# Optimization experiments

Measured on AMD Instinct MI355X. Metric: run time of the kernel, lower is better.

Reference implementation:

```python
import jax, jax.numpy as jnp
import numpy as np

B, IC, ID, OC, OD = 8, 8, 16, 8, 16   # batch, in_caps, in_dim, out_caps, out_dim
H = W = 32
K, STRIDE, PAD = 3, 1, 1
ITER = 3
EPS_BN = 1e-5
EPS_SQ = 1e-8


def p4convp4(x, w, stride, pad):
    """Group-equivariant P4->P4 conv.
    x: (N, Cin, 4, H, W); w: (Cout, Cin, 4, k, k) -> (N, Cout, 4, H', W').
    Output-rotation-r filter: input group axis rolled by r, spatial kernel rotated by r*90deg.
    """
    Cout, Cin, _, kh, kw = w.shape
    tw = jnp.stack(
        [jnp.rot90(jnp.roll(w, r, axis=2), k=r, axes=(3, 4)) for r in range(4)], axis=1
    )  # (Cout, 4, Cin, 4, k, k)
    tw = tw.reshape(Cout * 4, Cin * 4, kh, kw)
    N, _, _, Hh, Ww = x.shape
    xf = x.reshape(N, Cin * 4, Hh, Ww)
    y = jax.lax.conv_general_dilated(
        xf, tw, (stride, stride), [(pad, pad), (pad, pad)],
        dimension_numbers=("NCHW", "OIHW", "NCHW"))
    return y.reshape(N, Cout, 4, y.shape[2], y.shape[3])


def batchnorm3d(x, gamma, beta):
    # x: (N, C, D, H, W); training-mode batch stats over (N, D, H, W) per channel
    mean = x.mean(axis=(0, 2, 3, 4), keepdims=True)
    var = x.var(axis=(0, 2, 3, 4), keepdims=True)
    g = gamma.reshape(1, -1, 1, 1, 1)
    b = beta.reshape(1, -1, 1, 1, 1)
    return (x - mean) * jax.lax.rsqrt(var + EPS_BN) * g + b


def squash(s, axis):
    norm = jnp.linalg.norm(s, axis=axis, keepdims=True)
    scale = norm ** 2 / (1 + norm ** 2) / (norm + EPS_SQ)
    return scale * s


def setup_inputs() -> dict:
    key = jax.random.key(0)
    k1, k2 = jax.random.split(key)
    in_capsules = jax.random.normal(k1, (B, IC, ID, 4, H, W), jnp.float32)
    w = jax.random.normal(k2, (OC * OD, ID, 4, K, K), jnp.float32) * 0.05
    gamma = jnp.ones((OC * OD,), jnp.float32)
    beta = jnp.zeros((OC * OD,), jnp.float32)
    return {"in_capsules": in_capsules, "w": w, "gamma": gamma, "beta": beta}


def reference(in_capsules, w, gamma, beta):
    bsz = in_capsules.shape[0]
    x = in_capsules.reshape(bsz * IC, ID, 4, H, W)
    p = p4convp4(x, w, STRIDE, PAD)              # (B*IC, OC*OD, 4, H', W')
    p = batchnorm3d(p, gamma, beta)
    Hh, Ww = p.shape[-2], p.shape[-1]
    preds = p.reshape(bsz, IC, OC, OD, 4, Hh, Ww)

    b_ij = jnp.zeros((bsz, IC, OC, 1, 4, Hh, Ww), preds.dtype)
    c_ij = None
    v_j = None
    for it in range(ITER):
        c_ij = jax.nn.softmax(b_ij, axis=2)                      # over out_caps
        s_j = (c_ij * preds).sum(axis=1, keepdims=True)          # over in_caps
        v_j = squash(s_j, axis=3)                                # over out_dim
        if it < ITER - 1:
            b_ij = b_ij + (preds * v_j).sum(axis=3, keepdims=True)

    c = jnp.squeeze(c_ij, axis=3)                                # (B, IC, OC, 4, H', W')
    # normalized categorical entropy over out_caps
    ent = -(c * jnp.log(c)).sum(axis=2) / jnp.log(jnp.float32(OC))  # (B, IC, 4, H', W')
    entropy = ent.mean(axis=(1, 2, 3, 4)).sum()
    return (jnp.squeeze(v_j, axis=1), entropy)
```

## Files before the change

kernel.cpp:

```cpp
#include <hip/hip_runtime.h>
#include <hip/hip_bf16.h>


typedef short bf16x8 __attribute__((ext_vector_type(8)));
typedef float f32x4 __attribute__((ext_vector_type(4)));
typedef unsigned int u32x2 __attribute__((ext_vector_type(2)));

__device__ inline float bf2f(unsigned int u) {
    union { unsigned int i; float f; } x;
    x.i = u << 16;
    return x.f;
}
__device__ inline unsigned short f2bf(float f) {
    union { float f; unsigned int u; } x;
    x.f = f;
    unsigned int r = x.u + 0x7fffu + ((x.u >> 16) & 1u);
    return (unsigned short)(r >> 16);
}

__device__ inline float dppx1(float x) {
    return __int_as_float(__builtin_amdgcn_update_dpp(0, __float_as_int(x), 0xB1, 0xF, 0xF, false));
}
__device__ inline float dppx2(float x) {
    return __int_as_float(__builtin_amdgcn_update_dpp(0, __float_as_int(x), 0x4E, 0xF, 0xF, false));
}
template <int PATT>
__device__ inline float swzf(float x) {
    return __int_as_float(__builtin_amdgcn_ds_swizzle(__float_as_int(x), PATT));
}
#define SWZ4  0x101F
#define SWZ8  0x201F
#define SWZ16 0x401F
__device__ inline float psum32(float x) {
    u32x2 r = __builtin_amdgcn_permlane32_swap(__float_as_uint(x), __float_as_uint(x), false, false);
    return __uint_as_float(r[0]) + __uint_as_float(r[1]);
}

__global__ __launch_bounds__(256) void k_twb(const float* __restrict__ w,
                                             unsigned short* __restrict__ twb) {
    int idx = blockIdx.x * 256 + threadIdx.x;
    int tap = idx >> 15;
    int rem = idx & 32767;
    int co4 = rem >> 6;
    int cst = rem & 63;
    int ci = cst ^ ((co4 & 7) << 3);
    int r = co4 & 3, co = co4 >> 2;
    int s = ci & 3, cicap = ci >> 2;
    int ky = tap / 3, kx = tap % 3;
    int sy, sx;
    switch (r) {
        case 0: sy = ky;      sx = kx;      break;
        case 1: sy = kx;      sx = 2 - ky;  break;
        case 2: sy = 2 - ky;  sx = 2 - kx;  break;
        default: sy = 2 - kx; sx = ky;      break;
    }
    int ss = (s - r) & 3;
    twb[idx] = f2bf(w[(((co * 16 + cicap) * 4 + ss) * 3 + sy) * 3 + sx]);
}

__global__ __launch_bounds__(256) void k_prep(const float* __restrict__ xf,
                                              unsigned short* __restrict__ xpad) {
    int n = blockIdx.x >> 5, y = blockIdx.x & 31;
    int tid = threadIdx.x;
    __shared__ float tile[64][33];
#pragma unroll
    for (int it = 0; it < 8; ++it) {
        int ci = it * 8 + (tid >> 5), x = tid & 31;
        tile[ci][x] = xf[((n * 64 + ci) * 32 + y) * 32 + x];
    }
    __syncthreads();
    int xx = 1 + (tid >> 3), g = tid & 7;
    int x = xx - 1;
    int lg = g ^ (xx & 7);
    unsigned short vals[8];
#pragma unroll
    for (int j = 0; j < 8; ++j) vals[j] = f2bf(tile[lg * 8 + j][x]);
    uint4 pk;
    pk.x = (unsigned)vals[0] | ((unsigned)vals[1] << 16);
    pk.y = (unsigned)vals[2] | ((unsigned)vals[3] << 16);
    pk.z = (unsigned)vals[4] | ((unsigned)vals[5] << 16);
    pk.w = (unsigned)vals[6] | ((unsigned)vals[7] << 16);
    *reinterpret_cast<uint4*>(&xpad[(n * 34 + (y + 1)) * 2176 + xx * 64 + g * 8]) = pk;
}

__global__ __launch_bounds__(256) void k_mconv(const unsigned short* __restrict__ xpad,
                                               const unsigned short* __restrict__ twb,
                                               unsigned short* __restrict__ p) {
    int n = blockIdx.x, yt = blockIdx.y, cot = blockIdx.z;
    int y0 = yt * 4;
    int tid = threadIdx.x, lane = tid & 63, wave = tid >> 6;
    int wm = (wave >> 1) * 64, wn = (wave & 1) * 64;
    int p15 = lane & 15, hi = lane >> 4;

    __shared__ unsigned short xs[6 * 34 * 64];
    __shared__ unsigned short wA[128 * 64];

    {
        const uint4* src = reinterpret_cast<const uint4*>(xpad + (n * 34 + y0) * 2176);
        uint4* dst = reinterpret_cast<uint4*>(xs);
        for (int t = tid; t < 1632; t += 256) dst[t] = src[t];
    }

    f32x4 acc[4][4];
#pragma unroll
    for (int mf = 0; mf < 4; ++mf)
#pragma unroll
        for (int nf = 0; nf < 4; ++nf) acc[mf][nf] = (f32x4){0.f, 0.f, 0.f, 0.f};

    int yl[4], xb[4];
#pragma unroll
    for (int nf = 0; nf < 4; ++nf) {
        int posl = wn + nf * 16 + p15;
        yl[nf] = posl >> 5;
        xb[nf] = posl & 31;
    }

    for (int tap = 0; tap < 9; ++tap) {
        __syncthreads();
        {
            const uint4* wsrc = reinterpret_cast<const uint4*>(twb + (tap * 512 + cot * 128) * 64);
            uint4* wdst = reinterpret_cast<uint4*>(wA);
            for (int t = tid; t < 1024; t += 256) wdst[t] = wsrc[t];
        }
        __syncthreads();

        int ky = tap / 3, kx = tap % 3;

        bf16x8 a[4][2], b[4][2];
#pragma unroll
        for (int mf = 0; mf < 4; ++mf) {
            int co4l = wm + mf * 16 + p15;
#pragma unroll
            for (int s = 0; s < 2; ++s) {
                int cig = hi + s * 4;
                a[mf][s] = *reinterpret_cast<const bf16x8*>(
                    &wA[co4l * 64 + ((cig ^ (co4l & 7)) << 3)]);
            }
        }
#pragma unroll
        for (int nf = 0; nf < 4; ++nf) {
            int row = yl[nf] + ky, col = xb[nf] + kx;
#pragma unroll
            for (int s = 0; s < 2; ++s) {
                int cig = hi + s * 4;
                b[nf][s] = *reinterpret_cast<const bf16x8*>(
                    &xs[(row * 34 + col) * 64 + ((cig ^ (col & 7)) << 3)]);
            }
        }
#pragma unroll
        for (int s = 0; s < 2; ++s)
#pragma unroll
            for (int mf = 0; mf < 4; ++mf)
#pragma unroll
                for (int nf = 0; nf < 4; ++nf)
                    acc[mf][nf] = __builtin_amdgcn_mfma_f32_16x16x32_bf16(
                        a[mf][s], b[nf][s], acc[mf][nf], 0, 0, 0);
    }

#pragma unroll
    for (int mf = 0; mf < 4; ++mf)
#pragma unroll
        for (int nf = 0; nf < 4; ++nf) {
            int posl = wn + nf * 16 + p15;
            int y = y0 + (posl >> 5), x = posl & 31;
#pragma unroll
            for (int reg = 0; reg < 4; ++reg) {
                int co4 = cot * 128 + wm + mf * 16 + hi * 4 + reg;
                p[((n * 512 + co4) * 32 + y) * 32 + x] = f2bf(acc[mf][nf][reg]);
            }
        }
}

__global__ __launch_bounds__(256) void k_stats1(const unsigned short* __restrict__ pp,
                                                float* __restrict__ ps) {
    int c = blockIdx.x >> 2, q = blockIdx.x & 3;
    int tid = threadIdx.x;
    float s = 0.f, s2 = 0.f;
    for (int t = tid; t < 8192; t += 256) {
        int idx8 = t << 3;
        int nn = (q << 4) + (idx8 >> 12);
        int rem = idx8 & 4095;
        int co4 = (c << 2) + (rem >> 10);
        int pos = rem & 1023;
        uint4 d = *reinterpret_cast<const uint4*>(pp + (((nn << 9) + co4) << 10) + pos);
        float f;
        f = bf2f(d.x & 0xffffu); s += f; s2 += f * f;
        f = bf2f(d.x >> 16);     s += f; s2 += f * f;
        f = bf2f(d.y & 0xffffu); s += f; s2 += f * f;
        f = bf2f(d.y >> 16);     s += f; s2 += f * f;
        f = bf2f(d.z & 0xffffu); s += f; s2 += f * f;
        f = bf2f(d.z >> 16);     s += f; s2 += f * f;
        f = bf2f(d.w & 0xffffu); s += f; s2 += f * f;
        f = bf2f(d.w >> 16);     s += f; s2 += f * f;
    }
#pragma unroll
    for (int m = 1; m < 64; m <<= 1) {
        s  += __shfl_xor(s, m);
        s2 += __shfl_xor(s2, m);
    }
    __shared__ float rs[4], rs2[4];
    int wave = tid >> 6, lane = tid & 63;
    if (lane == 0) { rs[wave] = s; rs2[wave] = s2; }
    __syncthreads();
    if (tid == 0) {
        ps[blockIdx.x * 2]     = rs[0] + rs[1] + rs[2] + rs[3];
        ps[blockIdx.x * 2 + 1] = rs2[0] + rs2[1] + rs2[2] + rs2[3];
    }
}

__global__ __launch_bounds__(128) void k_ab(const float* __restrict__ ps,
                                            const float* __restrict__ gamma,
                                            const float* __restrict__ beta,
                                            float* __restrict__ ab) {
    int c = threadIdx.x;
    float S  = ps[(c * 4 + 0) * 2] + ps[(c * 4 + 1) * 2] + ps[(c * 4 + 2) * 2] + ps[(c * 4 + 3) * 2];
    float S2 = ps[(c * 4 + 0) * 2 + 1] + ps[(c * 4 + 1) * 2 + 1] + ps[(c * 4 + 2) * 2 + 1] + ps[(c * 4 + 3) * 2 + 1];
    float mean = S * (1.f / 262144.f);
    float var = S2 * (1.f / 262144.f) - mean * mean;
    float A = gamma[c] * rsqrtf(var + 1e-5f);
    ab[2 * c] = A;
    ab[2 * c + 1] = beta[c] - mean * A;
}

__global__ __launch_bounds__(256, 4) void k_route(const unsigned short* __restrict__ pp,
                                                  const float* __restrict__ ab,
                                                  float* __restrict__ out,
                                                  float* __restrict__ ent_out) {
    int bid = blockIdx.x;
    int u = ((bid >> 4) << 3) + (bid & 7);
    int ch = (bid >> 3) & 1;
    int y = u & 31, r = (u >> 5) & 3, b = u >> 7;
    int x0 = ch * 16;
    int tid = threadIdx.x;
    int wave = tid >> 6, lane = tid & 63;
    int i_l = lane >> 3, oc_l = lane & 7;

    __shared__ unsigned int Tl2[16][8][64];
    __shared__ unsigned short vst[8][16][18];
    __shared__ float ered[4];

#pragma unroll
    for (int t4i = 0; t4i < 4; ++t4i) {
        int t4 = tid + t4i * 256;
        int od = t4 >> 6, ls = t4 & 63;
        int ii = ls >> 3, oo = ls & 7;
        int c = oo * 16 + od;
        int co4 = c * 4 + r;
        int n = b * 8 + ii;
        float A = ab[2 * c], Bv = ab[2 * c + 1];
        const uint4* src = reinterpret_cast<const uint4*>(pp + ((n * 512 + co4) * 32 + y) * 32 + x0);
        uint4 d0 = src[0], d1 = src[1];
        unsigned wds[8] = {d0.x, d0.y, d0.z, d0.w, d1.x, d1.y, d1.z, d1.w};
#pragma unroll
        for (int j = 0; j < 8; ++j) {
            float tlo = A * bf2f(wds[j] & 0xffffu) + Bv;
            float thi = A * bf2f(wds[j] >> 16) + Bv;
            Tl2[od][j][ls] = (unsigned)f2bf(tlo) | ((unsigned)f2bf(thi) << 16);
        }
    }
    __syncthreads();

    float e_acc = 0.f;

    for (int q = 0; q < 2; ++q) {
        int p2 = wave + q * 4;
        float t0[16], t1[16];
#pragma unroll
        for (int od = 0; od < 16; ++od) {
            unsigned pr = Tl2[od][p2][lane];
            t0[od] = bf2f(pr & 0xffffu);
            t1[od] = bf2f(pr >> 16);
        }

        float b0 = 0.f, b1 = 0.f, c0, c1, sc0 = 0.f, sc1 = 0.f;
        float s0[16], s1[16];
        for (int it = 0; it < 3; ++it) {
            float m0 = b0, m1 = b1;
            m0 = fmaxf(m0, dppx1(m0));      m1 = fmaxf(m1, dppx1(m1));
            m0 = fmaxf(m0, dppx2(m0));      m1 = fmaxf(m1, dppx2(m1));
            m0 = fmaxf(m0, swzf<SWZ4>(m0)); m1 = fmaxf(m1, swzf<SWZ4>(m1));
            float e0 = __expf(b0 - m0), e1 = __expf(b1 - m1);
            float se0 = e0, se1 = e1;
            se0 += dppx1(se0);      se1 += dppx1(se1);
            se0 += dppx2(se0);      se1 += dppx2(se1);
            se0 += swzf<SWZ4>(se0); se1 += swzf<SWZ4>(se1);
            c0 = e0 * __builtin_amdgcn_rcpf(se0);
            c1 = e1 * __builtin_amdgcn_rcpf(se1);
            float n20 = 0.f, n21 = 0.f;
#pragma unroll
            for (int od = 0; od < 16; ++od) {
                float v0 = c0 * t0[od], v1 = c1 * t1[od];
                v0 += swzf<SWZ8>(v0);   v1 += swzf<SWZ8>(v1);
                v0 += swzf<SWZ16>(v0);  v1 += swzf<SWZ16>(v1);
                v0 = psum32(v0);        v1 = psum32(v1);
                s0[od] = v0;            s1[od] = v1;
                n20 += v0 * v0;         n21 += v1 * v1;
            }
            float nr0 = sqrtf(n20), nr1 = sqrtf(n21);
            sc0 = n20 * __builtin_amdgcn_rcpf((1.f + n20) * (nr0 + 1e-8f));
            sc1 = n21 * __builtin_amdgcn_rcpf((1.f + n21) * (nr1 + 1e-8f));
            if (it < 2) {
                float a0 = 0.f, a1 = 0.f;
#pragma unroll
                for (int od = 0; od < 16; ++od) {
                    a0 += t0[od] * s0[od];
                    a1 += t1[od] * s1[od];
                }
                b0 += a0 * sc0;
                b1 += a1 * sc1;
            }
        }
        e_acc += -c0 * __logf(c0) - c1 * __logf(c1);
        if (i_l == 0) {
#pragma unroll
            for (int od = 0; od < 16; ++od) {
                vst[oc_l][od][2 * p2]     = f2bf(sc0 * s0[od]);
                vst[oc_l][od][2 * p2 + 1] = f2bf(sc1 * s1[od]);
            }
        }
    }

    e_acc += dppx1(e_acc);
    e_acc += dppx2(e_acc);
    e_acc += swzf<SWZ4>(e_acc);
    e_acc += swzf<SWZ8>(e_acc);
    e_acc += swzf<SWZ16>(e_acc);
    e_acc = psum32(e_acc);
    if (lane == 0) ered[wave] = e_acc;
    __syncthreads();

    {
        int xx = tid & 15, od = (tid >> 4) & 15;
#pragma unroll
        for (int oc = 0; oc < 8; ++oc) {
            out[((((b * 8 + oc) * 16 + od) * 4 + r) * 32 + y) * 32 + x0 + xx] =
                bf2f(vst[oc][od][xx]);
        }
    }
    if (tid == 0) {
        float tot = ered[0] + ered[1] + ered[2] + ered[3];
        atomicAdd(ent_out, tot * (1.0f / (2.0794415416798357f * 32768.0f)));
    }
}

extern "C" void kernel_launch(void* const* d_in, const int* in_sizes, int n_in,
                              void* d_out, int out_size, void* d_ws, size_t ws_size,
                              hipStream_t stream) {
    const float* x     = (const float*)d_in[0];
    const float* w     = (const float*)d_in[1];
    const float* gamma = (const float*)d_in[2];
    const float* beta  = (const float*)d_in[3];
    float* out = (float*)d_out;

    char* ws = (char*)d_ws;
    unsigned short* p    = (unsigned short*)ws;
    unsigned short* xpad = (unsigned short*)(ws + 67108864);
    unsigned short* twb  = (unsigned short*)(ws + 67108864 + 9469952);
    float* ab            = (float*)(ws + 67108864 + 9469952 + 589824);
    float* ps            = (float*)(ws + 67108864 + 9469952 + 589824 + 1024);

    hipMemsetAsync(out + 4194304, 0, 4, stream);
    hipMemsetAsync(xpad, 0, 9469952, stream);

    k_twb<<<1152, 256, 0, stream>>>(w, twb);
    k_prep<<<2048, 256, 0, stream>>>(x, xpad);

    dim3 gconv(64, 8, 4);
    k_mconv<<<gconv, 256, 0, stream>>>(xpad, twb, p);

    k_stats1<<<512, 256, 0, stream>>>(p, ps);
    k_ab<<<1, 128, 0, stream>>>(ps, gamma, beta, ab);

    k_route<<<2048, 256, 0, stream>>>(p, ab, out, out + 4194304);
}
```

Measured before the change: 145.3 us.

## Fuse BN stats into conv, double-buffer weights via direct LDS loads, larger tile

The conv kernel now computes per-channel sum and sum-of-squares from its fp32 accumulators and adds them into a zeroed buffer with atomics. This removes the separate stats pass that re-read the whole 64MB bf16 intermediate. Weight taps are double-buffered and loaded with global_load_lds so the next tap's fetch overlaps the current MFMAs. The spatial tile grows from 4 to 8 rows per block, which doubles the accumulators per wave and raises register pressure. Stats are now taken from fp32 values rather than the rounded bf16 ones, and the atomic float summation order is nondeterministic.

```diff
diff --git a/kernel.cpp b/kernel.cpp
--- a/kernel.cpp
+++ b/kernel.cpp
@@ -16,6 +16,13 @@
     x.f = f;
     unsigned int r = x.u + 0x7fffu + ((x.u >> 16) & 1u);
     return (unsigned short)(r >> 16);
+}
+
+__device__ __forceinline__ void gld16(void* lds_uniform, const void* gsrc) {
+    __builtin_amdgcn_global_load_lds(
+        (const __attribute__((address_space(1))) unsigned int*)gsrc,
+        (__attribute__((address_space(3))) unsigned int*)lds_uniform,
+        16, 0, 0);
 }
 
 __device__ inline float dppx1(float x) {
@@ -83,128 +90,111 @@
     *reinterpret_cast<uint4*>(&xpad[(n * 34 + (y + 1)) * 2176 + xx * 64 + g * 8]) = pk;
 }
 
-__global__ __launch_bounds__(256) void k_mconv(const unsigned short* __restrict__ xpad,
-                                               const unsigned short* __restrict__ twb,
-                                               unsigned short* __restrict__ p) {
+__global__ __launch_bounds__(256, 2) void k_mconv(const unsigned short* __restrict__ xpad,
+                                                  const unsigned short* __restrict__ twb,
+                                                  unsigned short* __restrict__ p,
+                                                  float* __restrict__ ps) {
     int n = blockIdx.x, yt = blockIdx.y, cot = blockIdx.z;
-    int y0 = yt * 4;
+    int y0 = yt * 8;
     int tid = threadIdx.x, lane = tid & 63, wave = tid >> 6;
-    int wm = (wave >> 1) * 64, wn = (wave & 1) * 64;
+    int wm = (wave >> 1) * 64, wn = (wave & 1) * 128;
     int p15 = lane & 15, hi = lane >> 4;
 
-    __shared__ unsigned short xs[6 * 34 * 64];
-    __shared__ unsigned short wA[128 * 64];
+    __shared__ unsigned short xs[10 * 34 * 64];
+    __shared__ unsigned short wA[2][128 * 64];
 
     {
-        const uint4* src = reinterpret_cast<const uint4*>(xpad + (n * 34 + y0) * 2176);
-        uint4* dst = reinterpret_cast<uint4*>(xs);
-        for (int t = tid; t < 1632; t += 256) dst[t] = src[t];
-    }
-
-    f32x4 acc[4][4];
+        const unsigned short* xsrc = xpad + (n * 34 + y0) * 2176;
+#pragma unroll
+        for (int pass = 0; pass < 11; ++pass) {
+            int slot = pass * 256 + tid;
+            if (slot < 2720)
+                gld16(&xs[(pass * 256 + wave * 64) * 8], xsrc + slot * 8);
+        }
+        const unsigned short* wsrc = twb + (cot * 128) * 64;
+#pragma unroll
+        for (int pass = 0; pass < 4; ++pass)
+            gld16(&wA[0][(pass * 256 + wave * 64) * 8], wsrc + (pass * 256 + tid) * 8);
+    }
+    __syncthreads();
+
+    f32x4 acc[4][8];
 #pragma unroll
     for (int mf = 0; mf < 4; ++mf)
 #pragma unroll
-        for (int nf = 0; nf < 4; ++nf) acc[mf][nf] = (f32x4){0.f, 0.f, 0.f, 0.f};
-
-    int yl[4], xb[4];
-#pragma unroll
-    for (int nf = 0; nf < 4; ++nf) {
+        for (int nf = 0; nf < 8; ++nf) acc[mf][nf] = (f32x4){0.f, 0.f, 0.f, 0.f};
+
+    int yl[8], xb[8];
+#pragma unroll
+    for (int nf = 0; nf < 8; ++nf) {
         int posl = wn + nf * 16 + p15;
         yl[nf] = posl >> 5;
         xb[nf] = posl & 31;
     }
 
     for (int tap = 0; tap < 9; ++tap) {
+        int cb = tap & 1;
+        if (tap < 8) {
+            const unsigned short* wsrc = twb + ((tap + 1) * 512 + cot * 128) * 64;
+#pragma unroll
+            for (int pass = 0; pass < 4; ++pass)
+                gld16(&wA[cb ^ 1][(pass * 256 + wave * 64) * 8], wsrc + (pass * 256 + tid) * 8);
+        }
+        int ky = tap / 3, kx = tap % 3;
+
+#pragma unroll
+        for (int s = 0; s < 2; ++s) {
+            int cig = hi + s * 4;
+            bf16x8 a[4];
+#pragma unroll
+            for (int mf = 0; mf < 4; ++mf) {
+                int co4l = wm + mf * 16 + p15;
+                a[mf] = *reinterpret_cast<const bf16x8*>(
+                    &wA[cb][co4l * 64 + ((cig ^ (co4l & 7)) << 3)]);
+            }
+#pragma unroll
+            for (int nh = 0; nh < 2; ++nh) {
+                bf16x8 bfr[4];
+#pragma unroll
+                for (int nq = 0; nq < 4; ++nq) {
+                    int nf = nh * 4 + nq;
+                    int row = yl[nf] + ky, col = xb[nf] + kx;
+                    bfr[nq] = *reinterpret_cast<const bf16x8*>(
+                        &xs[(row * 34 + col) * 64 + ((cig ^ (col & 7)) << 3)]);
+                }
+#pragma unroll
+                for (int mf = 0; mf < 4; ++mf)
+#pragma unroll
+                    for (int nq = 0; nq < 4; ++nq)
+                        acc[mf][nh * 4 + nq] = __builtin_amdgcn_mfma_f32_16x16x32_bf16(
+                            a[mf], bfr[nq], acc[mf][nh * 4 + nq], 0, 0, 0);
+            }
+        }
         __syncthreads();
-        {
-            const uint4* wsrc = reinterpret_cast<const uint4*>(twb + (tap * 512 + cot * 128) * 64);
-            uint4* wdst = reinterpret_cast<uint4*>(wA);
-            for (int t = tid; t < 1024; t += 256) wdst[t] = wsrc[t];
-        }
-        __syncthreads();
-
-        int ky = tap / 3, kx = tap % 3;
-
-        bf16x8 a[4][2], b[4][2];
-#pragma unroll
-        for (int mf = 0; mf < 4; ++mf) {
-            int co4l = wm + mf * 16 + p15;
-#pragma unroll
-            for (int s = 0; s < 2; ++s) {
-                int cig = hi + s * 4;
-                a[mf][s] = *reinterpret_cast<const bf16x8*>(
-                    &wA[co4l * 64 + ((cig ^ (co4l & 7)) << 3)]);
-            }
-        }
-#pragma unroll
-        for (int nf = 0; nf < 4; ++nf) {
-            int row = yl[nf] + ky, col = xb[nf] + kx;
-#pragma unroll
-            for (int s = 0; s < 2; ++s) {
-                int cig = hi + s * 4;
-                b[nf][s] = *reinterpret_cast<const bf16x8*>(
-                    &xs[(row * 34 + col) * 64 + ((cig ^ (col & 7)) << 3)]);
-            }
-        }
-#pragma unroll
-        for (int s = 0; s < 2; ++s)
-#pragma unroll
-            for (int mf = 0; mf < 4; ++mf)
-#pragma unroll
-                for (int nf = 0; nf < 4; ++nf)
-                    acc[mf][nf] = __builtin_amdgcn_mfma_f32_16x16x32_bf16(
-                        a[mf][s], b[nf][s], acc[mf][nf], 0, 0, 0);
-    }
-
-#pragma unroll
-    for (int mf = 0; mf < 4; ++mf)
-#pragma unroll
-        for (int nf = 0; nf < 4; ++nf) {
+    }
+
+#pragma unroll
+    for (int mf = 0; mf < 4; ++mf) {
+        float s = 0.f, s2 = 0.f;
+#pragma unroll
+        for (int nf = 0; nf < 8; ++nf) {
             int posl = wn + nf * 16 + p15;
             int y = y0 + (posl >> 5), x = posl & 31;
 #pragma unroll
             for (int reg = 0; reg < 4; ++reg) {
+                float v = acc[mf][nf][reg];
+                s += v; s2 += v * v;
                 int co4 = cot * 128 + wm + mf * 16 + hi * 4 + reg;
-                p[((n * 512 + co4) * 32 + y) * 32 + x] = f2bf(acc[mf][nf][reg]);
-            }
-        }
-}
-
-__global__ __launch_bounds__(256) void k_stats1(const unsigned short* __restrict__ pp,
-                                                float* __restrict__ ps) {
-    int c = blockIdx.x >> 2, q = blockIdx.x & 3;
-    int tid = threadIdx.x;
-    float s = 0.f, s2 = 0.f;
-    for (int t = tid; t < 8192; t += 256) {
-        int idx8 = t << 3;
-        int nn = (q << 4) + (idx8 >> 12);
-        int rem = idx8 & 4095;
-        int co4 = (c << 2) + (rem >> 10);
-        int pos = rem & 1023;
-        uint4 d = *reinterpret_cast<const uint4*>(pp + (((nn << 9) + co4) << 10) + pos);
-        float f;
-        f = bf2f(d.x & 0xffffu); s += f; s2 += f * f;
-        f = bf2f(d.x >> 16);     s += f; s2 += f * f;
-        f = bf2f(d.y & 0xffffu); s += f; s2 += f * f;
-        f = bf2f(d.y >> 16);     s += f; s2 += f * f;
-        f = bf2f(d.z & 0xffffu); s += f; s2 += f * f;
-        f = bf2f(d.z >> 16);     s += f; s2 += f * f;
-        f = bf2f(d.w & 0xffffu); s += f; s2 += f * f;
-        f = bf2f(d.w >> 16);     s += f; s2 += f * f;
-    }
-#pragma unroll
-    for (int m = 1; m < 64; m <<= 1) {
-        s  += __shfl_xor(s, m);
-        s2 += __shfl_xor(s2, m);
-    }
-    __shared__ float rs[4], rs2[4];
-    int wave = tid >> 6, lane = tid & 63;
-    if (lane == 0) { rs[wave] = s; rs2[wave] = s2; }
-    __syncthreads();
-    if (tid == 0) {
-        ps[blockIdx.x * 2]     = rs[0] + rs[1] + rs[2] + rs[3];
-        ps[blockIdx.x * 2 + 1] = rs2[0] + rs2[1] + rs2[2] + rs2[3];
+                p[((n * 512 + co4) * 32 + y) * 32 + x] = f2bf(v);
+            }
+        }
+        s  += __shfl_xor(s, 1);  s  += __shfl_xor(s, 2);  s  += __shfl_xor(s, 4);  s  += __shfl_xor(s, 8);
+        s2 += __shfl_xor(s2, 1); s2 += __shfl_xor(s2, 2); s2 += __shfl_xor(s2, 4); s2 += __shfl_xor(s2, 8);
+        if (p15 == 0) {
+            int ch = cot * 32 + (wm >> 2) + mf * 4 + hi;
+            atomicAdd(&ps[2 * ch], s);
+            atomicAdd(&ps[2 * ch + 1], s2);
+        }
     }
 }
 
@@ -213,8 +203,8 @@
                                             const float* __restrict__ beta,
                                             float* __restrict__ ab) {
     int c = threadIdx.x;
-    float S  = ps[(c * 4 + 0) * 2] + ps[(c * 4 + 1) * 2] + ps[(c * 4 + 2) * 2] + ps[(c * 4 + 3) * 2];
-    float S2 = ps[(c * 4 + 0) * 2 + 1] + ps[(c * 4 + 1) * 2 + 1] + ps[(c * 4 + 2) * 2 + 1] + ps[(c * 4 + 3) * 2 + 1];
+    float S  = ps[2 * c];
+    float S2 = ps[2 * c + 1];
     float mean = S * (1.f / 262144.f);
     float var = S2 * (1.f / 262144.f) - mean * mean;
     float A = gamma[c] * rsqrtf(var + 1e-5f);
@@ -361,14 +351,14 @@
 
     hipMemsetAsync(out + 4194304, 0, 4, stream);
     hipMemsetAsync(xpad, 0, 9469952, stream);
+    hipMemsetAsync(ps, 0, 1024, stream);
 
     k_twb<<<1152, 256, 0, stream>>>(w, twb);
     k_prep<<<2048, 256, 0, stream>>>(x, xpad);
 
-    dim3 gconv(64, 8, 4);
-    k_mconv<<<gconv, 256, 0, stream>>>(xpad, twb, p);
-
-    k_stats1<<<512, 256, 0, stream>>>(p, ps);
+    dim3 gconv(64, 4, 4);
+    k_mconv<<<gconv, 256, 0, stream>>>(xpad, twb, p, ps);
+
     k_ab<<<1, 128, 0, stream>>>(ps, gamma, beta, ab);
 
     k_route<<<2048, 256, 0, stream>>>(p, ab, out, out + 4194304);
```

After: 188.6 us. +29.8%, slower.

## Relayout conv output so routing loads are contiguous per pixel row

Applied to the files above, without the earlier changes.

The conv kernel now writes its bf16 output in a layout indexed by rotation, row and half-row, then sample and channel, so each routing block reads one contiguous chunk instead of many scattered 32-byte pieces. The stats kernel is rewritten to stream contiguous chunks and emit per-block, per-channel partials. The affine-coefficient kernel now sums 512 partials per channel. Conv launch bounds add a minimum-occupancy hint of 3. The conv epilogue's stores become 32-byte scattered writes, and the final stats reduction is more serial.

```diff
diff --git a/kernel.cpp b/kernel.cpp
--- a/kernel.cpp
+++ b/kernel.cpp
@@ -83,9 +83,9 @@
     *reinterpret_cast<uint4*>(&xpad[(n * 34 + (y + 1)) * 2176 + xx * 64 + g * 8]) = pk;
 }
 
-__global__ __launch_bounds__(256) void k_mconv(const unsigned short* __restrict__ xpad,
-                                               const unsigned short* __restrict__ twb,
-                                               unsigned short* __restrict__ p) {
+__global__ __launch_bounds__(256, 3) void k_mconv(const unsigned short* __restrict__ xpad,
+                                                  const unsigned short* __restrict__ twb,
+                                                  unsigned short* __restrict__ p2) {
     int n = blockIdx.x, yt = blockIdx.y, cot = blockIdx.z;
     int y0 = yt * 4;
     int tid = threadIdx.x, lane = tid & 63, wave = tid >> 6;
@@ -158,31 +158,30 @@
     }
 
 #pragma unroll
-    for (int mf = 0; mf < 4; ++mf)
+    for (int mf = 0; mf < 4; ++mf) {
+        int c = cot * 32 + (wm >> 2) + mf * 4 + hi;
 #pragma unroll
         for (int nf = 0; nf < 4; ++nf) {
             int posl = wn + nf * 16 + p15;
-            int y = y0 + (posl >> 5), x = posl & 31;
+            int y = y0 + (posl >> 5);
+            int ch = (posl >> 4) & 1;
 #pragma unroll
             for (int reg = 0; reg < 4; ++reg) {
-                int co4 = cot * 128 + wm + mf * 16 + hi * 4 + reg;
-                p[((n * 512 + co4) * 32 + y) * 32 + x] = f2bf(acc[mf][nf][reg]);
-            }
-        }
+                int idx = ((((reg * 32 + y) * 2 + ch) * 64 + n) * 128 + c) * 16 + p15;
+                p2[idx] = f2bf(acc[mf][nf][reg]);
+            }
+        }
+    }
 }
 
 __global__ __launch_bounds__(256) void k_stats1(const unsigned short* __restrict__ pp,
                                                 float* __restrict__ ps) {
-    int c = blockIdx.x >> 2, q = blockIdx.x & 3;
-    int tid = threadIdx.x;
+    int blk = blockIdx.x, tid = threadIdx.x;
+    const uint4* base = reinterpret_cast<const uint4*>(pp) + blk * 8192;
     float s = 0.f, s2 = 0.f;
-    for (int t = tid; t < 8192; t += 256) {
-        int idx8 = t << 3;
-        int nn = (q << 4) + (idx8 >> 12);
-        int rem = idx8 & 4095;
-        int co4 = (c << 2) + (rem >> 10);
-        int pos = rem & 1023;
-        uint4 d = *reinterpret_cast<const uint4*>(pp + (((nn << 9) + co4) << 10) + pos);
+#pragma unroll 4
+    for (int k = 0; k < 32; ++k) {
+        uint4 d = base[k * 256 + tid];
         float f;
         f = bf2f(d.x & 0xffffu); s += f; s2 += f * f;
         f = bf2f(d.x >> 16);     s += f; s2 += f * f;
@@ -193,33 +192,34 @@
         f = bf2f(d.w & 0xffffu); s += f; s2 += f * f;
         f = bf2f(d.w >> 16);     s += f; s2 += f * f;
     }
-#pragma unroll
-    for (int m = 1; m < 64; m <<= 1) {
-        s  += __shfl_xor(s, m);
-        s2 += __shfl_xor(s2, m);
-    }
-    __shared__ float rs[4], rs2[4];
-    int wave = tid >> 6, lane = tid & 63;
-    if (lane == 0) { rs[wave] = s; rs2[wave] = s2; }
-    __syncthreads();
-    if (tid == 0) {
-        ps[blockIdx.x * 2]     = rs[0] + rs[1] + rs[2] + rs[3];
-        ps[blockIdx.x * 2 + 1] = rs2[0] + rs2[1] + rs2[2] + rs2[3];
-    }
-}
-
-__global__ __launch_bounds__(128) void k_ab(const float* __restrict__ ps,
+    s  += __shfl_xor(s, 1);
+    s2 += __shfl_xor(s2, 1);
+    if ((tid & 1) == 0) {
+        int c = tid >> 1;
+        ps[(blk * 128 + c) * 2]     = s;
+        ps[(blk * 128 + c) * 2 + 1] = s2;
+    }
+}
+
+__global__ __launch_bounds__(256) void k_ab(const float* __restrict__ ps,
                                             const float* __restrict__ gamma,
                                             const float* __restrict__ beta,
                                             float* __restrict__ ab) {
-    int c = threadIdx.x;
-    float S  = ps[(c * 4 + 0) * 2] + ps[(c * 4 + 1) * 2] + ps[(c * 4 + 2) * 2] + ps[(c * 4 + 3) * 2];
-    float S2 = ps[(c * 4 + 0) * 2 + 1] + ps[(c * 4 + 1) * 2 + 1] + ps[(c * 4 + 2) * 2 + 1] + ps[(c * 4 + 3) * 2 + 1];
-    float mean = S * (1.f / 262144.f);
-    float var = S2 * (1.f / 262144.f) - mean * mean;
-    float A = gamma[c] * rsqrtf(var + 1e-5f);
-    ab[2 * c] = A;
-    ab[2 * c + 1] = beta[c] - mean * A;
+    int c = threadIdx.x >> 1, h = threadIdx.x & 1;
+    float S = 0.f, S2 = 0.f;
+    for (int b = h * 256; b < h * 256 + 256; ++b) {
+        S  += ps[(b * 128 + c) * 2];
+        S2 += ps[(b * 128 + c) * 2 + 1];
+    }
+    S  += __shfl_xor(S, 1);
+    S2 += __shfl_xor(S2, 1);
+    if (h == 0) {
+        float mean = S * (1.f / 262144.f);
+        float var = S2 * (1.f / 262144.f) - mean * mean;
+        float A = gamma[c] * rsqrtf(var + 1e-5f);
+        ab[2 * c] = A;
+        ab[2 * c + 1] = beta[c] - mean * A;
+    }
 }
 
 __global__ __launch_bounds__(256, 4) void k_route(const unsigned short* __restrict__ pp,
@@ -239,23 +239,22 @@
     __shared__ unsigned short vst[8][16][18];
     __shared__ float ered[4];
 
-#pragma unroll
-    for (int t4i = 0; t4i < 4; ++t4i) {
-        int t4 = tid + t4i * 256;
-        int od = t4 >> 6, ls = t4 & 63;
-        int ii = ls >> 3, oo = ls & 7;
-        int c = oo * 16 + od;
-        int co4 = c * 4 + r;
-        int n = b * 8 + ii;
+    const uint4* src = reinterpret_cast<const uint4*>(pp) +
+                       (((((r * 32 + y) * 2 + ch) * 64) + b * 8) << 8);
+#pragma unroll
+    for (int pass = 0; pass < 8; ++pass) {
+        int slot = pass * 256 + tid;
+        int il = slot >> 8, c = (slot >> 1) & 127, half = slot & 1;
+        int od = c & 15, oo = c >> 4;
+        int ls = il * 8 + oo;
         float A = ab[2 * c], Bv = ab[2 * c + 1];
-        const uint4* src = reinterpret_cast<const uint4*>(pp + ((n * 512 + co4) * 32 + y) * 32 + x0);
-        uint4 d0 = src[0], d1 = src[1];
-        unsigned wds[8] = {d0.x, d0.y, d0.z, d0.w, d1.x, d1.y, d1.z, d1.w};
-#pragma unroll
-        for (int j = 0; j < 8; ++j) {
-            float tlo = A * bf2f(wds[j] & 0xffffu) + Bv;
-            float thi = A * bf2f(wds[j] >> 16) + Bv;
-            Tl2[od][j][ls] = (unsigned)f2bf(tlo) | ((unsigned)f2bf(thi) << 16);
+        uint4 d = src[slot];
+        unsigned wds[4] = {d.x, d.y, d.z, d.w};
+#pragma unroll
+        for (int jj = 0; jj < 4; ++jj) {
+            float tlo = A * bf2f(wds[jj] & 0xffffu) + Bv;
+            float thi = A * bf2f(wds[jj] >> 16) + Bv;
+            Tl2[od][half * 4 + jj][ls] = (unsigned)f2bf(tlo) | ((unsigned)f2bf(thi) << 16);
         }
     }
     __syncthreads();
@@ -263,11 +262,11 @@
     float e_acc = 0.f;
 
     for (int q = 0; q < 2; ++q) {
-        int p2 = wave + q * 4;
+        int p2i = wave + q * 4;
         float t0[16], t1[16];
 #pragma unroll
         for (int od = 0; od < 16; ++od) {
-            unsigned pr = Tl2[od][p2][lane];
+            unsigned pr = Tl2[od][p2i][lane];
             t0[od] = bf2f(pr & 0xffffu);
             t1[od] = bf2f(pr >> 16);
         }
@@ -314,8 +313,8 @@
         if (i_l == 0) {
 #pragma unroll
             for (int od = 0; od < 16; ++od) {
-                vst[oc_l][od][2 * p2]     = f2bf(sc0 * s0[od]);
-                vst[oc_l][od][2 * p2 + 1] = f2bf(sc1 * s1[od]);
+                vst[oc_l][od][2 * p2i]     = f2bf(sc0 * s0[od]);
+                vst[oc_l][od][2 * p2i + 1] = f2bf(sc1 * s1[od]);
             }
         }
     }
@@ -353,7 +352,7 @@
     float* out = (float*)d_out;
 
     char* ws = (char*)d_ws;
-    unsigned short* p    = (unsigned short*)ws;
+    unsigned short* p2   = (unsigned short*)ws;
     unsigned short* xpad = (unsigned short*)(ws + 67108864);
     unsigned short* twb  = (unsigned short*)(ws + 67108864 + 9469952);
     float* ab            = (float*)(ws + 67108864 + 9469952 + 589824);
@@ -366,10 +365,10 @@
     k_prep<<<2048, 256, 0, stream>>>(x, xpad);
 
     dim3 gconv(64, 8, 4);
-    k_mconv<<<gconv, 256, 0, stream>>>(xpad, twb, p);
-
-    k_stats1<<<512, 256, 0, stream>>>(p, ps);
-    k_ab<<<1, 128, 0, stream>>>(ps, gamma, beta, ab);
-
-    k_route<<<2048, 256, 0, stream>>>(p, ab, out, out + 4194304);
-}
+    k_mconv<<<gconv, 256, 0, stream>>>(xpad, twb, p2);
+
+    k_stats1<<<512, 256, 0, stream>>>(p2, ps);
+    k_ab<<<1, 256, 0, stream>>>(ps, gamma, beta, ab);
+
+    k_route<<<2048, 256, 0, stream>>>(p2, ab, out, out + 4194304);
+}
```

After: 167.0 us. +15.0%, slower.
